# Kernel optimization log

Hardware: AMD Instinct MI355X
Metric: run time of the kernel (lower is better)

## Reference

```python
import jax, jax.numpy as jnp
import numpy as np

PE_DIM = 40  # pe_dim; gaussian PE scale factor = pe_dim // 2


def _batched_linear(x, wb):
    # x: [B, N, D], wb: [B, D+1, H] (last row is bias)
    return jnp.einsum('bnd,bdh->bnh', x, wb[:, :-1, :]) + wb[:, -1:, :]


def setup_inputs() -> dict:
    key = jax.random.key(0)
    ks = jax.random.split(key, 8)
    B, N = 16, 16384
    H = 256
    pe_out = 3 * PE_DIM  # 120
    s = 0.05  # keep ReLU-chain activations bounded
    return {
        'x': jax.random.normal(ks[0], (B, N, 3), dtype=jnp.float32),
        'wb0': jax.random.normal(ks[1], (B, pe_out + 1, H), dtype=jnp.float32) * s,
        'wb1': jax.random.normal(ks[2], (B, H + 1, H), dtype=jnp.float32) * s,
        'wb2': jax.random.normal(ks[3], (B, H + 1, H), dtype=jnp.float32) * s,
        'wb3': jax.random.normal(ks[4], (B, H + 1, H), dtype=jnp.float32) * s,
        'wb4': jax.random.normal(ks[5], (B, H + 1, H), dtype=jnp.float32) * s,
        'wb_out': jax.random.normal(ks[6], (B, H + 1, 1), dtype=jnp.float32) * s,
        'rand_freqs': jax.random.normal(ks[7], (3 * (PE_DIM // 2), 3), dtype=jnp.float32),  # feat_sigma=1
    }


def reference(x, wb0, wb1, wb2, wb3, wb4, wb_out, rand_freqs):
    # Gaussian positional encoding: k = x . (rand_freqs * pe_dim//2)
    k = jnp.einsum('bnd,fd->bnf', x, rand_freqs * (PE_DIM // 2))  # [B,N,60]
    h = jnp.concatenate([jnp.sin(k), jnp.cos(k)], axis=-1)        # [B,N,120]
    for wb in (wb0, wb1, wb2, wb3, wb4):
        h = jax.nn.relu(_batched_linear(h, wb))
    out = _batched_linear(h, wb_out)  # [B,N,1]
    return out
```

## Files before the change

kernel.cpp:

```cpp
#include <hip/hip_runtime.h>
#include <hip/hip_bf16.h>


#define H 256
#define MT 128
#define PE_NF 60

typedef __attribute__((ext_vector_type(8))) short s16x8;
typedef __attribute__((ext_vector_type(4))) float f32x4;

static __device__ __forceinline__ unsigned short f2bf(float v) {
  unsigned int u = __float_as_uint(v);
  return (unsigned short)((u + 0x7FFFu + ((u >> 16) & 1u)) >> 16);
}
static __device__ __forceinline__ float bf2f(unsigned short u) {
  return __uint_as_float(((unsigned int)u) << 16);
}
static __device__ __forceinline__ int hswz(int row, int chunk) {
  return (chunk & ~7) | ((chunk ^ row) & 7);
}

__global__ __launch_bounds__(256) void prep_weights(
    const float* __restrict__ wb0, const float* __restrict__ wb1,
    const float* __restrict__ wb2, const float* __restrict__ wb3,
    const float* __restrict__ wb4,
    unsigned short* __restrict__ w0t, unsigned short* __restrict__ w14t,
    float* __restrict__ biases) {
  int z = blockIdx.z;
  int li = z >> 4, b = z & 15;
  int k0 = blockIdx.x * 32;
  int n0 = blockIdx.y * 32;
  int Ks, Kd;
  const float* src;
  unsigned short* dst;
  if (li == 0) {
    Ks = 120; Kd = 128;
    if (k0 >= 128) return;
    src = wb0 + (size_t)b * 121 * H;
    dst = w0t + (size_t)b * H * 128;
  } else {
    Ks = 256; Kd = 256;
    const float* srcs[4] = {wb1, wb2, wb3, wb4};
    src = srcs[li - 1] + (size_t)b * 257 * H;
    dst = w14t + ((size_t)(li - 1) * 16 + b) * H * 256;
  }
  __shared__ float tile[32][33];
  int tx = threadIdx.x & 31, ty0 = threadIdx.x >> 5;
#pragma unroll
  for (int i = 0; i < 4; ++i) {
    int k = k0 + ty0 + i * 8;
    tile[ty0 + i * 8][tx] = (k < Ks) ? src[(size_t)k * H + n0 + tx] : 0.f;
  }
  if (k0 == 0 && ty0 == 0)
    biases[((size_t)li * 16 + b) * H + n0 + tx] = src[(size_t)Ks * H + n0 + tx];
  __syncthreads();
#pragma unroll
  for (int i = 0; i < 4; ++i) {
    int n = n0 + ty0 + i * 8;
    dst[(size_t)n * Kd + k0 + tx] = f2bf(tile[tx][ty0 + i * 8]);
  }
}

template <int NKT>
static __device__ __forceinline__ void mlp_layer(
    const unsigned short* __restrict__ wl, const float* __restrict__ bl,
    unsigned short* __restrict__ h_s, const int rlane, const int kgrp,
    const int w) {
  const int n_base = w * 64;

  f32x4 acc[8][4];
  {
    f32x4 bini[4];
#pragma unroll
    for (int ct = 0; ct < 4; ++ct)
      bini[ct] = *(const f32x4*)(bl + n_base + ct * 16 + kgrp * 4);
#pragma unroll
    for (int rt = 0; rt < 8; ++rt)
#pragma unroll
      for (int ct = 0; ct < 4; ++ct) acc[rt][ct] = bini[ct];
  }

  const unsigned short* wp[4];
#pragma unroll
  for (int ct = 0; ct < 4; ++ct)
    wp[ct] = wl + (size_t)(n_base + ct * 16 + rlane) * (NKT * 32) + kgrp * 8;
  int aoff[8];
#pragma unroll
  for (int rt = 0; rt < 8; ++rt) aoff[rt] = (rt * 16 + rlane) * 256;

  s16x8 bb[2][4];
#pragma unroll
  for (int ct = 0; ct < 4; ++ct) bb[0][ct] = *(const s16x8*)(wp[ct]);

#pragma unroll
  for (int kt = 0; kt < NKT; ++kt) {
    if (kt + 1 < NKT) {
#pragma unroll
      for (int ct = 0; ct < 4; ++ct)
        bb[(kt + 1) & 1][ct] = *(const s16x8*)(wp[ct] + (kt + 1) * 32);
    }
    s16x8 afr[8];
    const int cs = hswz(rlane, kt * 4 + kgrp) * 8;
#pragma unroll
    for (int rt = 0; rt < 8; ++rt)
      afr[rt] = *(const s16x8*)&h_s[aoff[rt] + cs];
#pragma unroll
    for (int rt = 0; rt < 8; ++rt)
#pragma unroll
      for (int ct = 0; ct < 4; ++ct)
        acc[rt][ct] = __builtin_amdgcn_mfma_f32_16x16x32_bf16(
            bb[kt & 1][ct], afr[rt], acc[rt][ct], 0, 0, 0);
  }
  __syncthreads();

  const int sub = (kgrp & 1) * 4;
  const int cbase = w * 8 + (kgrp >> 1);
#pragma unroll
  for (int rt = 0; rt < 8; ++rt) {
    const int m = rt * 16 + rlane;
    const int rowb = m * 256;
#pragma unroll
    for (int ct = 0; ct < 4; ++ct) {
      const int cs = hswz(m, cbase + ct * 2);
      float v0 = fmaxf(acc[rt][ct][0], 0.f);
      float v1 = fmaxf(acc[rt][ct][1], 0.f);
      float v2 = fmaxf(acc[rt][ct][2], 0.f);
      float v3 = fmaxf(acc[rt][ct][3], 0.f);
      union { __hip_bfloat162 h2[2]; uint2 u; } pk;
      pk.h2[0] = __float22bfloat162_rn(float2{v0, v1});
      pk.h2[1] = __float22bfloat162_rn(float2{v2, v3});
      *(uint2*)&h_s[rowb + cs * 8 + sub] = pk.u;
    }
  }
  __syncthreads();
}

__global__ __launch_bounds__(256, 2) void hyponerf_main(
    const float* __restrict__ x, const float* __restrict__ rfreq,
    const float* __restrict__ wbout,
    const unsigned short* __restrict__ w0t, const unsigned short* __restrict__ w14t,
    const float* __restrict__ biases, float* __restrict__ out) {
  __shared__ __align__(16) unsigned short h_s[MT * 256];
  __shared__ float fr_s[PE_NF * 3];
  __shared__ float x_s[MT * 3];
  __shared__ float wout_s[H + 1];

  int bid = blockIdx.x;
  int logical = (bid & 7) * 256 + (bid >> 3);
  int b  = logical >> 7;
  int mt = logical & 127;

  int t = threadIdx.x;
  int w = t >> 6, l = t & 63;
  int rlane = l & 15;
  int kgrp  = l >> 4;

  const float* xg = x + ((size_t)b * 16384 + (size_t)mt * MT) * 3;
  for (int i = t; i < MT * 3; i += 256) x_s[i] = xg[i];
  for (int i = t; i < PE_NF * 3; i += 256) fr_s[i] = rfreq[i] * 20.0f;
  for (int i = t; i < H + 1; i += 256) wout_s[i] = wbout[(size_t)b * (H + 1) + i];
  __syncthreads();

  {
    int r = t >> 1;
    int fb = (t & 1) * 30;
    float x0 = x_s[r * 3 + 0], x1 = x_s[r * 3 + 1], x2 = x_s[r * 3 + 2];
    int rowb = r * 256;
#pragma unroll
    for (int j = 0; j < 30; ++j) {
      int f = fb + j;
      float kv = x0 * fr_s[f * 3 + 0] + x1 * fr_s[f * 3 + 1] + x2 * fr_s[f * 3 + 2];
      float sv, cv;
      __sincosf(kv, &sv, &cv);
      h_s[rowb + hswz(r, f >> 3) * 8 + (f & 7)] = f2bf(sv);
      int g = 60 + f;
      h_s[rowb + hswz(r, g >> 3) * 8 + (g & 7)] = f2bf(cv);
    }
    if ((t & 1) == 0) {
      int cs = hswz(r, 15) * 8;
#pragma unroll
      for (int p = 0; p < 8; ++p) h_s[rowb + cs + p] = 0;
    }
  }
  __syncthreads();

  mlp_layer<4>(w0t + (size_t)b * H * 128, biases + (size_t)b * H, h_s,
               rlane, kgrp, w);
#pragma unroll 1
  for (int li = 1; li < 5; ++li) {
    mlp_layer<8>(w14t + ((size_t)(li - 1) * 16 + b) * H * 256,
                 biases + ((size_t)li * 16 + b) * H, h_s, rlane, kgrp, w);
  }

  {
    int r = t >> 1;
    int cb = (t & 1) * 16;
    int rowb = r * 256;
    float sum = 0.f;
#pragma unroll
    for (int c = 0; c < 16; ++c) {
      int ch = cb + c;
      const s16x8 hv = *(const s16x8*)&h_s[rowb + hswz(r, ch) * 8];
#pragma unroll
      for (int j = 0; j < 8; ++j)
        sum += bf2f((unsigned short)hv[j]) * wout_s[ch * 8 + j];
    }
    sum += __shfl_xor(sum, 1);
    if ((t & 1) == 0)
      out[(size_t)b * 16384 + (size_t)mt * MT + r] = sum + wout_s[H];
  }
}

extern "C" void kernel_launch(void* const* d_in, const int* in_sizes, int n_in,
                              void* d_out, int out_size, void* d_ws, size_t ws_size,
                              hipStream_t stream) {
  const float* x     = (const float*)d_in[0];
  const float* wb0   = (const float*)d_in[1];
  const float* wb1   = (const float*)d_in[2];
  const float* wb2   = (const float*)d_in[3];
  const float* wb3   = (const float*)d_in[4];
  const float* wb4   = (const float*)d_in[5];
  const float* wbout = (const float*)d_in[6];
  const float* rfreq = (const float*)d_in[7];
  float* out = (float*)d_out;

  char* ws = (char*)d_ws;
  unsigned short* w0t  = (unsigned short*)ws;
  unsigned short* w14t = (unsigned short*)(ws + (size_t)16 * 256 * 128 * 2);
  float* biases = (float*)(ws + (size_t)16 * 256 * 128 * 2
                              + (size_t)4 * 16 * 256 * 256 * 2);

  prep_weights<<<dim3(8, 8, 80), 256, 0, stream>>>(wb0, wb1, wb2, wb3, wb4,
                                                   w0t, w14t, biases);
  hyponerf_main<<<dim3(2048), 256, 0, stream>>>(x, rfreq, wbout, w0t, w14t,
                                                biases, out);
}
```

Measured before the change: 193.8 us.

## Halve row tile to 64, raise occupancy to 3 blocks/CU, vectorize PE writes

Shrinks the per-block row tile from 128 to 64, which halves the accumulator registers and LDS use so three blocks can share a CU, and doubles the grid to 4096 blocks. The PE stage now has each thread build whole 8-element chunks and write them with one vector store, and the output dot product is split across four threads. It also raises wave priority around the MFMA bursts. In exchange, each weight tile fetched from global or L2 is reused over half as many rows, so weight traffic per output roughly doubles.

```diff
diff --git a/kernel.cpp b/kernel.cpp
--- a/kernel.cpp
+++ b/kernel.cpp
@@ -3,7 +3,7 @@
 
 
 #define H 256
-#define MT 128
+#define MT 64
 #define PE_NF 60
 
 typedef __attribute__((ext_vector_type(8))) short s16x8;
@@ -68,14 +68,14 @@
     const int w) {
   const int n_base = w * 64;
 
-  f32x4 acc[8][4];
+  f32x4 acc[4][4];
   {
     f32x4 bini[4];
 #pragma unroll
     for (int ct = 0; ct < 4; ++ct)
       bini[ct] = *(const f32x4*)(bl + n_base + ct * 16 + kgrp * 4);
 #pragma unroll
-    for (int rt = 0; rt < 8; ++rt)
+    for (int rt = 0; rt < 4; ++rt)
 #pragma unroll
       for (int ct = 0; ct < 4; ++ct) acc[rt][ct] = bini[ct];
   }
@@ -84,9 +84,9 @@
 #pragma unroll
   for (int ct = 0; ct < 4; ++ct)
     wp[ct] = wl + (size_t)(n_base + ct * 16 + rlane) * (NKT * 32) + kgrp * 8;
-  int aoff[8];
-#pragma unroll
-  for (int rt = 0; rt < 8; ++rt) aoff[rt] = (rt * 16 + rlane) * 256;
+  int aoff[4];
+#pragma unroll
+  for (int rt = 0; rt < 4; ++rt) aoff[rt] = (rt * 16 + rlane) * 256;
 
   s16x8 bb[2][4];
 #pragma unroll
@@ -99,24 +99,26 @@
       for (int ct = 0; ct < 4; ++ct)
         bb[(kt + 1) & 1][ct] = *(const s16x8*)(wp[ct] + (kt + 1) * 32);
     }
-    s16x8 afr[8];
+    s16x8 afr[4];
     const int cs = hswz(rlane, kt * 4 + kgrp) * 8;
 #pragma unroll
-    for (int rt = 0; rt < 8; ++rt)
+    for (int rt = 0; rt < 4; ++rt)
       afr[rt] = *(const s16x8*)&h_s[aoff[rt] + cs];
-#pragma unroll
-    for (int rt = 0; rt < 8; ++rt)
+    __builtin_amdgcn_s_setprio(1);
+#pragma unroll
+    for (int rt = 0; rt < 4; ++rt)
 #pragma unroll
       for (int ct = 0; ct < 4; ++ct)
         acc[rt][ct] = __builtin_amdgcn_mfma_f32_16x16x32_bf16(
             bb[kt & 1][ct], afr[rt], acc[rt][ct], 0, 0, 0);
+    __builtin_amdgcn_s_setprio(0);
   }
   __syncthreads();
 
   const int sub = (kgrp & 1) * 4;
   const int cbase = w * 8 + (kgrp >> 1);
 #pragma unroll
-  for (int rt = 0; rt < 8; ++rt) {
+  for (int rt = 0; rt < 4; ++rt) {
     const int m = rt * 16 + rlane;
     const int rowb = m * 256;
 #pragma unroll
@@ -135,7 +137,7 @@
   __syncthreads();
 }
 
-__global__ __launch_bounds__(256, 2) void hyponerf_main(
+__global__ __launch_bounds__(256, 3) void hyponerf_main(
     const float* __restrict__ x, const float* __restrict__ rfreq,
     const float* __restrict__ wbout,
     const unsigned short* __restrict__ w0t, const unsigned short* __restrict__ w14t,
@@ -146,9 +148,9 @@
   __shared__ float wout_s[H + 1];
 
   int bid = blockIdx.x;
-  int logical = (bid & 7) * 256 + (bid >> 3);
-  int b  = logical >> 7;
-  int mt = logical & 127;
+  int logical = (bid & 7) * 512 + (bid >> 3);
+  int b  = logical >> 8;
+  int mt = logical & 255;
 
   int t = threadIdx.x;
   int w = t >> 6, l = t & 63;
@@ -162,24 +164,28 @@
   __syncthreads();
 
   {
-    int r = t >> 1;
-    int fb = (t & 1) * 30;
+    int r = t >> 2;
+    int q = t & 3;
     float x0 = x_s[r * 3 + 0], x1 = x_s[r * 3 + 1], x2 = x_s[r * 3 + 2];
     int rowb = r * 256;
 #pragma unroll
-    for (int j = 0; j < 30; ++j) {
-      int f = fb + j;
-      float kv = x0 * fr_s[f * 3 + 0] + x1 * fr_s[f * 3 + 1] + x2 * fr_s[f * 3 + 2];
-      float sv, cv;
-      __sincosf(kv, &sv, &cv);
-      h_s[rowb + hswz(r, f >> 3) * 8 + (f & 7)] = f2bf(sv);
-      int g = 60 + f;
-      h_s[rowb + hswz(r, g >> 3) * 8 + (g & 7)] = f2bf(cv);
-    }
-    if ((t & 1) == 0) {
-      int cs = hswz(r, 15) * 8;
-#pragma unroll
-      for (int p = 0; p < 8; ++p) h_s[rowb + cs + p] = 0;
+    for (int cc = 0; cc < 4; ++cc) {
+      union { unsigned short us[8]; s16x8 v; } pk;
+#pragma unroll
+      for (int j = 0; j < 8; ++j) {
+        int n = q * 32 + cc * 8 + j;
+        float v = 0.f;
+        if (n < 60) {
+          float kv = x0 * fr_s[n * 3] + x1 * fr_s[n * 3 + 1] + x2 * fr_s[n * 3 + 2];
+          v = __sinf(kv);
+        } else if (n < 120) {
+          int f = n - 60;
+          float kv = x0 * fr_s[f * 3] + x1 * fr_s[f * 3 + 1] + x2 * fr_s[f * 3 + 2];
+          v = __cosf(kv);
+        }
+        pk.us[j] = f2bf(v);
+      }
+      *(s16x8*)&h_s[rowb + hswz(r, q * 4 + cc) * 8] = pk.v;
     }
   }
   __syncthreads();
@@ -193,20 +199,21 @@
   }
 
   {
-    int r = t >> 1;
-    int cb = (t & 1) * 16;
+    int r = t >> 2;
+    int q = t & 3;
     int rowb = r * 256;
     float sum = 0.f;
 #pragma unroll
-    for (int c = 0; c < 16; ++c) {
-      int ch = cb + c;
+    for (int c = 0; c < 8; ++c) {
+      int ch = q * 8 + c;
       const s16x8 hv = *(const s16x8*)&h_s[rowb + hswz(r, ch) * 8];
 #pragma unroll
       for (int j = 0; j < 8; ++j)
         sum += bf2f((unsigned short)hv[j]) * wout_s[ch * 8 + j];
     }
     sum += __shfl_xor(sum, 1);
-    if ((t & 1) == 0)
+    sum += __shfl_xor(sum, 2);
+    if (q == 0)
       out[(size_t)b * 16384 + (size_t)mt * MT + r] = sum + wout_s[H];
   }
 }
@@ -232,6 +239,6 @@
 
   prep_weights<<<dim3(8, 8, 80), 256, 0, stream>>>(wb0, wb1, wb2, wb3, wb4,
                                                    w0t, w14t, biases);
-  hyponerf_main<<<dim3(2048), 256, 0, stream>>>(x, rfreq, wbout, w0t, w14t,
+  hyponerf_main<<<dim3(4096), 256, 0, stream>>>(x, rfreq, wbout, w0t, w14t,
                                                 biases, out);
 }
```

New measurement: 294.5 us. 51.9% more time.

## Pre-pack weights in MFMA fragment order and prefetch across layers

Applied to the files above, without the earlier changes.

The weight prep kernel now writes bf16 weights in a fragment-packed layout, so each lane's B-fragment load is one contiguous 16-byte access that coalesces across the wavefront instead of a strided row read. The first fragment of the next layer is prefetched during the last k-step of the current layer, and the layer loop is fully unrolled so the register ping-pong buffer carries over between layers. MFMA blocks are wrapped in s_setprio to favor matrix issue. The positional-encoding stage now writes 16-byte vector stores, at the cost of computing both sin and cos separately per element.

```diff
diff --git a/kernel.cpp b/kernel.cpp
--- a/kernel.cpp
+++ b/kernel.cpp
@@ -24,48 +24,56 @@
     const float* __restrict__ wb0, const float* __restrict__ wb1,
     const float* __restrict__ wb2, const float* __restrict__ wb3,
     const float* __restrict__ wb4,
-    unsigned short* __restrict__ w0t, unsigned short* __restrict__ w14t,
+    unsigned short* __restrict__ w0p, unsigned short* __restrict__ w14p,
     float* __restrict__ biases) {
   int z = blockIdx.z;
   int li = z >> 4, b = z & 15;
   int k0 = blockIdx.x * 32;
   int n0 = blockIdx.y * 32;
-  int Ks, Kd;
+  int Ks;
   const float* src;
   unsigned short* dst;
   if (li == 0) {
-    Ks = 120; Kd = 128;
+    Ks = 120;
     if (k0 >= 128) return;
     src = wb0 + (size_t)b * 121 * H;
-    dst = w0t + (size_t)b * H * 128;
+    dst = w0p + (size_t)b * 32768;
   } else {
-    Ks = 256; Kd = 256;
+    Ks = 256;
     const float* srcs[4] = {wb1, wb2, wb3, wb4};
     src = srcs[li - 1] + (size_t)b * 257 * H;
-    dst = w14t + ((size_t)(li - 1) * 16 + b) * H * 256;
+    dst = w14p + ((size_t)(li - 1) * 16 + b) * 65536;
   }
   __shared__ float tile[32][33];
-  int tx = threadIdx.x & 31, ty0 = threadIdx.x >> 5;
+  int t = threadIdx.x;
+  int tx = t & 31, ty = t >> 5;
 #pragma unroll
   for (int i = 0; i < 4; ++i) {
-    int k = k0 + ty0 + i * 8;
-    tile[ty0 + i * 8][tx] = (k < Ks) ? src[(size_t)k * H + n0 + tx] : 0.f;
-  }
-  if (k0 == 0 && ty0 == 0)
+    int k = k0 + ty + i * 8;
+    tile[ty + i * 8][tx] = (k < Ks) ? src[(size_t)k * H + n0 + tx] : 0.f;
+  }
+  if (k0 == 0 && ty == 0)
     biases[((size_t)li * 16 + b) * H + n0 + tx] = src[(size_t)Ks * H + n0 + tx];
   __syncthreads();
-#pragma unroll
-  for (int i = 0; i < 4; ++i) {
-    int n = n0 + ty0 + i * 8;
-    dst[(size_t)n * Kd + k0 + tx] = f2bf(tile[tx][ty0 + i * 8]);
-  }
-}
-
-template <int NKT>
+  if (t < 128) {
+    int nn = t & 31, kg = t >> 5;
+    int n = n0 + nn;
+    int kt = k0 >> 5;
+    int w = n >> 6, ct = (n >> 4) & 3, rl = n & 15;
+    union { unsigned short us[8]; s16x8 v; } pk;
+#pragma unroll
+    for (int j = 0; j < 8; ++j) pk.us[j] = f2bf(tile[kg * 8 + j][nn]);
+    *(s16x8*)&dst[(size_t)(kt * 16 + w * 4 + ct) * 512 + (kg * 16 + rl) * 8] = pk.v;
+  }
+}
+
+template <int NKT, bool LAST>
 static __device__ __forceinline__ void mlp_layer(
-    const unsigned short* __restrict__ wl, const float* __restrict__ bl,
-    unsigned short* __restrict__ h_s, const int rlane, const int kgrp,
-    const int w) {
+    const unsigned short* __restrict__ wl, const unsigned short* __restrict__ wln,
+    const float* __restrict__ bl, unsigned short* __restrict__ h_s,
+    const int rlane, const int kgrp, const int w, const int l,
+    s16x8 (&bb)[2][4]) {
+  static_assert((NKT & 1) == 0, "ping-pong parity needs even NKT");
   const int n_base = w * 64;
 
   f32x4 acc[8][4];
@@ -80,36 +88,36 @@
       for (int ct = 0; ct < 4; ++ct) acc[rt][ct] = bini[ct];
   }
 
-  const unsigned short* wp[4];
-#pragma unroll
-  for (int ct = 0; ct < 4; ++ct)
-    wp[ct] = wl + (size_t)(n_base + ct * 16 + rlane) * (NKT * 32) + kgrp * 8;
+  const unsigned short* fp = wl + (size_t)(w * 4) * 512 + l * 8;
   int aoff[8];
 #pragma unroll
   for (int rt = 0; rt < 8; ++rt) aoff[rt] = (rt * 16 + rlane) * 256;
-
-  s16x8 bb[2][4];
-#pragma unroll
-  for (int ct = 0; ct < 4; ++ct) bb[0][ct] = *(const s16x8*)(wp[ct]);
 
 #pragma unroll
   for (int kt = 0; kt < NKT; ++kt) {
     if (kt + 1 < NKT) {
 #pragma unroll
       for (int ct = 0; ct < 4; ++ct)
-        bb[(kt + 1) & 1][ct] = *(const s16x8*)(wp[ct] + (kt + 1) * 32);
+        bb[(kt + 1) & 1][ct] = *(const s16x8*)(fp + (kt + 1) * 8192 + ct * 512);
+    } else if (!LAST) {
+      const unsigned short* fpn = wln + (size_t)(w * 4) * 512 + l * 8;
+#pragma unroll
+      for (int ct = 0; ct < 4; ++ct)
+        bb[0][ct] = *(const s16x8*)(fpn + ct * 512);
     }
     s16x8 afr[8];
     const int cs = hswz(rlane, kt * 4 + kgrp) * 8;
 #pragma unroll
     for (int rt = 0; rt < 8; ++rt)
       afr[rt] = *(const s16x8*)&h_s[aoff[rt] + cs];
+    __builtin_amdgcn_s_setprio(1);
 #pragma unroll
     for (int rt = 0; rt < 8; ++rt)
 #pragma unroll
       for (int ct = 0; ct < 4; ++ct)
         acc[rt][ct] = __builtin_amdgcn_mfma_f32_16x16x32_bf16(
             bb[kt & 1][ct], afr[rt], acc[rt][ct], 0, 0, 0);
+    __builtin_amdgcn_s_setprio(0);
   }
   __syncthreads();
 
@@ -138,7 +146,7 @@
 __global__ __launch_bounds__(256, 2) void hyponerf_main(
     const float* __restrict__ x, const float* __restrict__ rfreq,
     const float* __restrict__ wbout,
-    const unsigned short* __restrict__ w0t, const unsigned short* __restrict__ w14t,
+    const unsigned short* __restrict__ w0p, const unsigned short* __restrict__ w14p,
     const float* __restrict__ biases, float* __restrict__ out) {
   __shared__ __align__(16) unsigned short h_s[MT * 256];
   __shared__ float fr_s[PE_NF * 3];
@@ -155,6 +163,19 @@
   int rlane = l & 15;
   int kgrp  = l >> 4;
 
+  const unsigned short* wl0 = w0p + (size_t)b * 32768;
+  const unsigned short* wl1 = w14p + (size_t)(0 * 16 + b) * 65536;
+  const unsigned short* wl2 = w14p + (size_t)(1 * 16 + b) * 65536;
+  const unsigned short* wl3 = w14p + (size_t)(2 * 16 + b) * 65536;
+  const unsigned short* wl4 = w14p + (size_t)(3 * 16 + b) * 65536;
+
+  s16x8 bb[2][4];
+  {
+    const unsigned short* fp0 = wl0 + (size_t)(w * 4) * 512 + l * 8;
+#pragma unroll
+    for (int ct = 0; ct < 4; ++ct) bb[0][ct] = *(const s16x8*)(fp0 + ct * 512);
+  }
+
   const float* xg = x + ((size_t)b * 16384 + (size_t)mt * MT) * 3;
   for (int i = t; i < MT * 3; i += 256) x_s[i] = xg[i];
   for (int i = t; i < PE_NF * 3; i += 256) fr_s[i] = rfreq[i] * 20.0f;
@@ -163,34 +184,41 @@
 
   {
     int r = t >> 1;
-    int fb = (t & 1) * 30;
+    int q = t & 1;
     float x0 = x_s[r * 3 + 0], x1 = x_s[r * 3 + 1], x2 = x_s[r * 3 + 2];
     int rowb = r * 256;
 #pragma unroll
-    for (int j = 0; j < 30; ++j) {
-      int f = fb + j;
-      float kv = x0 * fr_s[f * 3 + 0] + x1 * fr_s[f * 3 + 1] + x2 * fr_s[f * 3 + 2];
-      float sv, cv;
-      __sincosf(kv, &sv, &cv);
-      h_s[rowb + hswz(r, f >> 3) * 8 + (f & 7)] = f2bf(sv);
-      int g = 60 + f;
-      h_s[rowb + hswz(r, g >> 3) * 8 + (g & 7)] = f2bf(cv);
-    }
-    if ((t & 1) == 0) {
-      int cs = hswz(r, 15) * 8;
-#pragma unroll
-      for (int p = 0; p < 8; ++p) h_s[rowb + cs + p] = 0;
-    }
-  }
-  __syncthreads();
-
-  mlp_layer<4>(w0t + (size_t)b * H * 128, biases + (size_t)b * H, h_s,
-               rlane, kgrp, w);
-#pragma unroll 1
-  for (int li = 1; li < 5; ++li) {
-    mlp_layer<8>(w14t + ((size_t)(li - 1) * 16 + b) * H * 256,
-                 biases + ((size_t)li * 16 + b) * H, h_s, rlane, kgrp, w);
-  }
+    for (int cc = 0; cc < 8; ++cc) {
+      union { unsigned short us[8]; s16x8 v; } pk;
+#pragma unroll
+      for (int j = 0; j < 8; ++j) {
+        int n = q * 64 + cc * 8 + j;
+        float v = 0.f;
+        if (n < 60) {
+          float kv = x0 * fr_s[n * 3] + x1 * fr_s[n * 3 + 1] + x2 * fr_s[n * 3 + 2];
+          v = __sinf(kv);
+        } else if (n < 120) {
+          int f = n - 60;
+          float kv = x0 * fr_s[f * 3] + x1 * fr_s[f * 3 + 1] + x2 * fr_s[f * 3 + 2];
+          v = __cosf(kv);
+        }
+        pk.us[j] = f2bf(v);
+      }
+      *(s16x8*)&h_s[rowb + hswz(r, q * 8 + cc) * 8] = pk.v;
+    }
+  }
+  __syncthreads();
+
+  mlp_layer<4, false>(wl0, wl1, biases + (size_t)(0 * 16 + b) * H, h_s,
+                      rlane, kgrp, w, l, bb);
+  mlp_layer<8, false>(wl1, wl2, biases + (size_t)(1 * 16 + b) * H, h_s,
+                      rlane, kgrp, w, l, bb);
+  mlp_layer<8, false>(wl2, wl3, biases + (size_t)(2 * 16 + b) * H, h_s,
+                      rlane, kgrp, w, l, bb);
+  mlp_layer<8, false>(wl3, wl4, biases + (size_t)(3 * 16 + b) * H, h_s,
+                      rlane, kgrp, w, l, bb);
+  mlp_layer<8, true >(wl4, wl4, biases + (size_t)(4 * 16 + b) * H, h_s,
+                      rlane, kgrp, w, l, bb);
 
   {
     int r = t >> 1;
@@ -225,13 +253,13 @@
   float* out = (float*)d_out;
 
   char* ws = (char*)d_ws;
-  unsigned short* w0t  = (unsigned short*)ws;
-  unsigned short* w14t = (unsigned short*)(ws + (size_t)16 * 256 * 128 * 2);
-  float* biases = (float*)(ws + (size_t)16 * 256 * 128 * 2
-                              + (size_t)4 * 16 * 256 * 256 * 2);
+  unsigned short* w0p  = (unsigned short*)ws;
+  unsigned short* w14p = (unsigned short*)(ws + (size_t)16 * 32768 * 2);
+  float* biases = (float*)(ws + (size_t)16 * 32768 * 2
+                              + (size_t)64 * 65536 * 2);
 
   prep_weights<<<dim3(8, 8, 80), 256, 0, stream>>>(wb0, wb1, wb2, wb3, wb4,
-                                                   w0t, w14t, biases);
-  hyponerf_main<<<dim3(2048), 256, 0, stream>>>(x, rfreq, wbout, w0t, w14t,
+                                                   w0p, w14p, biases);
+  hyponerf_main<<<dim3(2048), 256, 0, stream>>>(x, rfreq, wbout, w0p, w14p,
                                                 biases, out);
 }
```

Result: faster. 173.3 us (-10.6%).
